# Kernel tuning notes

Hardware: AMD Instinct MI355X
Metric: run time of the kernel (lower is better)

Reference implementation:

```python
import jax, jax.numpy as jnp
import numpy as np

S, B, C = 7, 2, 20
LAMBDA_COORD, LAMBDA_NOOBJ = 5.0, 0.5
N_BATCH = 8192
OBJ_PROB = 0.05


def setup_inputs() -> dict:
    key = jax.random.key(0)
    k_pred, k_tgt, k_obj = jax.random.split(key, 3)
    pred = jax.random.normal(k_pred, (N_BATCH, S * S * (5 * B + C)), dtype=jnp.float32)
    # target cells: [conf, x, y, w, h, 20 class scores]; conf must be exactly 0/1
    tgt = jax.random.uniform(k_tgt, (N_BATCH * S * S, 5 + C), dtype=jnp.float32)
    obj = jax.random.bernoulli(k_obj, OBJ_PROB, (N_BATCH * S * S,)).astype(jnp.float32)
    tgt = tgt.at[:, 0].set(obj)
    target = tgt.reshape(N_BATCH, S * S * (5 + C))
    return {"pred": pred, "target": target}


def _to_xyxy(xywh, gy, gx):
    # xywh: [..., 4]; gy/gx broadcastable to leading dims
    cx = (gx + xywh[..., 0]) / S
    cy = (gy + xywh[..., 1]) / S
    w = xywh[..., 2]
    h = xywh[..., 3]
    return jnp.stack([cx - w / 2, cy - h / 2, cx + w / 2, cy + h / 2], axis=-1)


def _yolo_loss(pred, target):
    N = pred.shape[0]
    p = pred.reshape(-1, 5 * B + C)          # [M, 30], M = N*S*S
    t = target.reshape(-1, 5 + C)            # [M, 25]
    M = p.shape[0]
    objf = (t[:, 0] == 1.0).astype(p.dtype)
    noobjf = (t[:, 0] == 0.0).astype(p.dtype)

    boxes = p[:, : 5 * B].reshape(M, B, 5)   # [M, B, 5] (conf, x, y, w, h)
    tbox = t[:, :5]                           # [M, 5]

    grid = jnp.tile(jnp.arange(S * S), M // (S * S))
    gy = (grid // 7).astype(p.dtype)
    gx = (grid % 7).astype(p.dtype)

    # IoU matching (pred wh taken as abs, matching .square().sqrt())
    pb = jnp.abs(boxes[..., 1:5])                             # [M, B, 4]
    pxyxy = _to_xyxy(pb, gy[:, None], gx[:, None])            # [M, B, 4]
    txyxy = _to_xyxy(tbox[:, 1:5], gy, gx)                    # [M, 4]

    lt = jnp.maximum(pxyxy[..., :2], txyxy[:, None, :2])
    rb = jnp.minimum(pxyxy[..., 2:], txyxy[:, None, 2:])
    wh = jnp.clip(rb - lt, 0.0)
    inter = wh[..., 0] * wh[..., 1]                           # [M, B]
    area_p = (pxyxy[..., 2] - pxyxy[..., 0]) * (pxyxy[..., 3] - pxyxy[..., 1])
    area_t = (txyxy[..., 2] - txyxy[..., 0]) * (txyxy[..., 3] - txyxy[..., 1])
    iou = inter / (area_p + area_t[:, None] - inter)          # [M, B]

    best = jnp.argmax(iou, axis=1)                            # first max on ties, like torch
    max_iou = jnp.max(iou, axis=1)                            # [M]
    resp = jnp.take_along_axis(boxes, best[:, None, None], axis=1)[:, 0]  # [M, 5]

    # localization (raw pred xy; sqrt(abs(wh)))
    xy_loss = jnp.sum(objf[:, None] * (resp[:, 1:3] - tbox[:, 1:3]) ** 2)
    pw = jnp.sqrt(jnp.abs(resp[:, 3:5]))
    tw = jnp.sqrt(jnp.abs(tbox[:, 3:5]))
    wh_loss = jnp.sum(objf[:, None] * (pw - tw) ** 2)
    localization = LAMBDA_COORD * (xy_loss + wh_loss)

    # confidence: responsible box conf vs IoU (IoU NOT detached, as in source)
    obj_conf = jnp.sum(objf * (resp[:, 0] - max_iou) ** 2)
    noobj_conf = LAMBDA_NOOBJ * jnp.sum(noobjf[:, None] * boxes[:, :, 0] ** 2)

    cls_loss = jnp.sum(objf[:, None] * (p[:, -C:] - t[:, -C:]) ** 2)

    return (localization + obj_conf + noobj_conf + cls_loss) / N


def reference(pred, target):
    return _yolo_loss(pred, target)
```

## Files before the change

kernel.cpp:

```cpp
#include <hip/hip_runtime.h>


#define NBATCH  8192
#define PSTRIDE 30
#define TSTRIDE 25
#define TPB     256
#define NCHUNKS 1568

__global__ __launch_bounds__(TPB) void yolo_partial_kernel(
    const float* __restrict__ pred,
    const float* __restrict__ tgt,
    float* __restrict__ partials)
{
    __shared__ float sp[TPB * PSTRIDE];
    __shared__ float st[TPB * TSTRIDE];

    const int tid = threadIdx.x;
    const size_t c0 = (size_t)blockIdx.x * TPB;

    const float4* gp = (const float4*)(pred + c0 * PSTRIDE);
    float4* lp = (float4*)sp;
    #pragma unroll
    for (int k = 0; k < 7; ++k)
        lp[tid + k * TPB] = gp[tid + k * TPB];
    if (tid < 128)
        lp[tid + 7 * TPB] = gp[tid + 7 * TPB];

    const float4* gt = (const float4*)(tgt + c0 * TSTRIDE);
    float4* lt = (float4*)st;
    #pragma unroll
    for (int k = 0; k < 6; ++k)
        lt[tid + k * TPB] = gt[tid + k * TPB];
    if (tid < 64)
        lt[tid + 6 * TPB] = gt[tid + 6 * TPB];

    __syncthreads();

    const float* p = sp + tid * PSTRIDE;
    const float* t = st + tid * TSTRIDE;

    int cell = (int)((c0 + tid) % 49);
    float gy = (float)(cell / 7);
    float gx = (float)(cell % 7);
    const float invS = 1.0f / 7.0f;

    float t0 = t[0], tx = t[1], ty = t[2], tw = t[3], th = t[4];
    float objf   = (t0 == 1.0f) ? 1.0f : 0.0f;
    float noobjf = (t0 == 0.0f) ? 1.0f : 0.0f;

    float tcx = (gx + tx) * invS, tcy = (gy + ty) * invS;
    float tx1 = tcx - tw * 0.5f, ty1 = tcy - th * 0.5f;
    float tx2 = tcx + tw * 0.5f, ty2 = tcy + th * 0.5f;
    float area_t = (tx2 - tx1) * (ty2 - ty1);

    float conf[2], bx[2], by[2], bw[2], bh[2], iou[2];
    #pragma unroll
    for (int b = 0; b < 2; ++b) {
        conf[b] = p[b * 5 + 0];
        bx[b]   = p[b * 5 + 1];
        by[b]   = p[b * 5 + 2];
        bw[b]   = p[b * 5 + 3];
        bh[b]   = p[b * 5 + 4];
        float ax = fabsf(bx[b]), ay = fabsf(by[b]);
        float aw = fabsf(bw[b]), ah = fabsf(bh[b]);
        float cx = (gx + ax) * invS, cy = (gy + ay) * invS;
        float x1 = cx - aw * 0.5f, y1 = cy - ah * 0.5f;
        float x2 = cx + aw * 0.5f, y2 = cy + ah * 0.5f;
        float ltx = fmaxf(x1, tx1), lty = fmaxf(y1, ty1);
        float rbx = fminf(x2, tx2), rby = fminf(y2, ty2);
        float wx = fmaxf(rbx - ltx, 0.0f);
        float wy = fmaxf(rby - lty, 0.0f);
        float inter = wx * wy;
        float area_p = (x2 - x1) * (y2 - y1);
        iou[b] = inter / (area_p + area_t - inter);
    }

    int best = (iou[1] > iou[0]) ? 1 : 0;
    float miou = fmaxf(iou[0], iou[1]);

    float rc = conf[best];
    float rx = bx[best], ry = by[best], rw = bw[best], rh = bh[best];

    float dx = rx - tx, dy = ry - ty;
    float sw = sqrtf(fabsf(rw)) - sqrtf(fabsf(tw));
    float sh = sqrtf(fabsf(rh)) - sqrtf(fabsf(th));
    float loc = dx * dx + dy * dy + sw * sw + sh * sh;

    float oc = rc - miou;
    oc = oc * oc;

    float no = conf[0] * conf[0] + conf[1] * conf[1];

    float cls = 0.0f;
    #pragma unroll
    for (int k = 0; k < 20; ++k) {
        float d = p[10 + k] - t[5 + k];
        cls += d * d;
    }

    float part = objf * (5.0f * loc + oc + cls) + 0.5f * noobjf * no;

    #pragma unroll
    for (int off = 32; off > 0; off >>= 1)
        part += __shfl_down(part, off, 64);

    __shared__ float ws[4];
    int lane = tid & 63;
    int wid  = tid >> 6;
    if (lane == 0) ws[wid] = part;
    __syncthreads();
    if (tid == 0)
        partials[blockIdx.x] = ws[0] + ws[1] + ws[2] + ws[3];
}

__global__ __launch_bounds__(TPB) void yolo_final_kernel(
    const float* __restrict__ partials,
    float* __restrict__ out, float invN)
{
    const int tid = threadIdx.x;
    float s = 0.0f;
    for (int i = tid; i < NCHUNKS; i += TPB)
        s += partials[i];

    #pragma unroll
    for (int off = 32; off > 0; off >>= 1)
        s += __shfl_down(s, off, 64);

    __shared__ float ws[4];
    int lane = tid & 63;
    int wid  = tid >> 6;
    if (lane == 0) ws[wid] = s;
    __syncthreads();
    if (tid == 0)
        out[0] = (ws[0] + ws[1] + ws[2] + ws[3]) * invN;
}

extern "C" void kernel_launch(void* const* d_in, const int* in_sizes, int n_in,
                              void* d_out, int out_size, void* d_ws, size_t ws_size,
                              hipStream_t stream) {
    const float* pred = (const float*)d_in[0];
    const float* tgt  = (const float*)d_in[1];
    float* out = (float*)d_out;
    float* partials = (float*)d_ws;

    yolo_partial_kernel<<<NCHUNKS, TPB, 0, stream>>>(pred, tgt, partials);
    yolo_final_kernel<<<1, TPB, 0, stream>>>(partials, out, 1.0f / (float)NBATCH);
}
```

Baseline: 25.20 us.

## Fuse partial and final reduction into one cooperative kernel with grid sync

Replaces the two-kernel reduction with a single cooperatively launched, persistent grid-stride kernel. Each block accumulates over several chunks, writes a partial, then a grid-wide barrier lets block 0 do the final sum. This removes the second kernel launch and its launch gap. The costs are the cooperative launch, the grid barrier, an occupancy query on every call, and a grid capped by per-CU occupancy (with 55KB of shared memory only about two blocks fit per CU). The old two-kernel path stays as a fallback.

```diff
diff --git a/kernel.cpp b/kernel.cpp
--- a/kernel.cpp
+++ b/kernel.cpp
@@ -1,4 +1,7 @@
 #include <hip/hip_runtime.h>
+#include <hip/hip_cooperative_groups.h>
+
+namespace cg = cooperative_groups;
 
 
 #define NBATCH  8192
@@ -7,39 +10,10 @@
 #define TPB     256
 #define NCHUNKS 1568
 
-__global__ __launch_bounds__(TPB) void yolo_partial_kernel(
-    const float* __restrict__ pred,
-    const float* __restrict__ tgt,
-    float* __restrict__ partials)
-{
-    __shared__ float sp[TPB * PSTRIDE];
-    __shared__ float st[TPB * TSTRIDE];
-
-    const int tid = threadIdx.x;
-    const size_t c0 = (size_t)blockIdx.x * TPB;
-
-    const float4* gp = (const float4*)(pred + c0 * PSTRIDE);
-    float4* lp = (float4*)sp;
-    #pragma unroll
-    for (int k = 0; k < 7; ++k)
-        lp[tid + k * TPB] = gp[tid + k * TPB];
-    if (tid < 128)
-        lp[tid + 7 * TPB] = gp[tid + 7 * TPB];
-
-    const float4* gt = (const float4*)(tgt + c0 * TSTRIDE);
-    float4* lt = (float4*)st;
-    #pragma unroll
-    for (int k = 0; k < 6; ++k)
-        lt[tid + k * TPB] = gt[tid + k * TPB];
-    if (tid < 64)
-        lt[tid + 6 * TPB] = gt[tid + 6 * TPB];
-
-    __syncthreads();
-
-    const float* p = sp + tid * PSTRIDE;
-    const float* t = st + tid * TSTRIDE;
-
-    int cell = (int)((c0 + tid) % 49);
+__device__ __forceinline__ float cell_loss(const float* __restrict__ p,
+                                           const float* __restrict__ t,
+                                           int cell)
+{
     float gy = (float)(cell / 7);
     float gx = (float)(cell % 7);
     const float invS = 1.0f / 7.0f;
@@ -98,37 +72,130 @@
         cls += d * d;
     }
 
-    float part = objf * (5.0f * loc + oc + cls) + 0.5f * noobjf * no;
+    return objf * (5.0f * loc + oc + cls) + 0.5f * noobjf * no;
+}
+
+__global__ __launch_bounds__(TPB) void yolo_fused_kernel(
+    const float* __restrict__ pred,
+    const float* __restrict__ tgt,
+    float* __restrict__ out,
+    float* __restrict__ partials, float invN)
+{
+    __shared__ float sp[TPB * PSTRIDE];
+    __shared__ float st[TPB * TSTRIDE];
+    __shared__ float ws[4];
+
+    const int tid = threadIdx.x;
+    float part = 0.0f;
+
+    for (int c = blockIdx.x; c < NCHUNKS; c += gridDim.x) {
+        const size_t c0 = (size_t)c * TPB;
+
+        const float4* gp = (const float4*)(pred + c0 * PSTRIDE);
+        float4* lp = (float4*)sp;
+        #pragma unroll
+        for (int k = 0; k < 7; ++k)
+            lp[tid + k * TPB] = gp[tid + k * TPB];
+        if (tid < 128)
+            lp[tid + 7 * TPB] = gp[tid + 7 * TPB];
+
+        const float4* gt = (const float4*)(tgt + c0 * TSTRIDE);
+        float4* lt = (float4*)st;
+        #pragma unroll
+        for (int k = 0; k < 6; ++k)
+            lt[tid + k * TPB] = gt[tid + k * TPB];
+        if (tid < 64)
+            lt[tid + 6 * TPB] = gt[tid + 6 * TPB];
+
+        __syncthreads();
+
+        part += cell_loss(sp + tid * PSTRIDE, st + tid * TSTRIDE,
+                          (int)((c0 + tid) % 49));
+
+        __syncthreads();
+    }
 
     #pragma unroll
     for (int off = 32; off > 0; off >>= 1)
         part += __shfl_down(part, off, 64);
-
-    __shared__ float ws[4];
-    int lane = tid & 63;
-    int wid  = tid >> 6;
+    int lane = tid & 63, wid = tid >> 6;
     if (lane == 0) ws[wid] = part;
     __syncthreads();
     if (tid == 0)
         partials[blockIdx.x] = ws[0] + ws[1] + ws[2] + ws[3];
+
+    cg::this_grid().sync();
+
+    if (blockIdx.x == 0) {
+        float s = 0.0f;
+        for (int i = tid; i < (int)gridDim.x; i += TPB)
+            s += partials[i];
+        #pragma unroll
+        for (int off = 32; off > 0; off >>= 1)
+            s += __shfl_down(s, off, 64);
+        if (lane == 0) ws[wid] = s;
+        __syncthreads();
+        if (tid == 0)
+            out[0] = (ws[0] + ws[1] + ws[2] + ws[3]) * invN;
+    }
+}
+
+__global__ __launch_bounds__(TPB) void yolo_partial_kernel(
+    const float* __restrict__ pred,
+    const float* __restrict__ tgt,
+    float* __restrict__ partials)
+{
+    __shared__ float sp[TPB * PSTRIDE];
+    __shared__ float st[TPB * TSTRIDE];
+
+    const int tid = threadIdx.x;
+    const size_t c0 = (size_t)blockIdx.x * TPB;
+
+    const float4* gp = (const float4*)(pred + c0 * PSTRIDE);
+    float4* lp = (float4*)sp;
+    #pragma unroll
+    for (int k = 0; k < 7; ++k)
+        lp[tid + k * TPB] = gp[tid + k * TPB];
+    if (tid < 128)
+        lp[tid + 7 * TPB] = gp[tid + 7 * TPB];
+
+    const float4* gt = (const float4*)(tgt + c0 * TSTRIDE);
+    float4* lt = (float4*)st;
+    #pragma unroll
+    for (int k = 0; k < 6; ++k)
+        lt[tid + k * TPB] = gt[tid + k * TPB];
+    if (tid < 64)
+        lt[tid + 6 * TPB] = gt[tid + 6 * TPB];
+
+    __syncthreads();
+
+    float part = cell_loss(sp + tid * PSTRIDE, st + tid * TSTRIDE,
+                           (int)((c0 + tid) % 49));
+
+    #pragma unroll
+    for (int off = 32; off > 0; off >>= 1)
+        part += __shfl_down(part, off, 64);
+    __shared__ float ws[4];
+    int lane = tid & 63, wid = tid >> 6;
+    if (lane == 0) ws[wid] = part;
+    __syncthreads();
+    if (tid == 0)
+        partials[blockIdx.x] = ws[0] + ws[1] + ws[2] + ws[3];
 }
 
 __global__ __launch_bounds__(TPB) void yolo_final_kernel(
     const float* __restrict__ partials,
-    float* __restrict__ out, float invN)
+    float* __restrict__ out, float invN, int n)
 {
     const int tid = threadIdx.x;
     float s = 0.0f;
-    for (int i = tid; i < NCHUNKS; i += TPB)
+    for (int i = tid; i < n; i += TPB)
         s += partials[i];
-
     #pragma unroll
     for (int off = 32; off > 0; off >>= 1)
         s += __shfl_down(s, off, 64);
-
     __shared__ float ws[4];
-    int lane = tid & 63;
-    int wid  = tid >> 6;
+    int lane = tid & 63, wid = tid >> 6;
     if (lane == 0) ws[wid] = s;
     __syncthreads();
     if (tid == 0)
@@ -142,7 +209,23 @@
     const float* tgt  = (const float*)d_in[1];
     float* out = (float*)d_out;
     float* partials = (float*)d_ws;
+    float invN = 1.0f / (float)NBATCH;
+
+    int perCU = 0;
+    hipError_t e = hipOccupancyMaxActiveBlocksPerMultiprocessor(
+        &perCU, (const void*)yolo_fused_kernel, TPB, 0);
+
+    if (e == hipSuccess && perCU > 0) {
+        int grid = perCU * 256;
+        if (grid > NCHUNKS) grid = NCHUNKS;
+        void* args[] = {(void*)&pred, (void*)&tgt, (void*)&out,
+                        (void*)&partials, (void*)&invN};
+        hipError_t e2 = hipLaunchCooperativeKernel(
+            (const void*)yolo_fused_kernel, dim3(grid), dim3(TPB),
+            args, 0, stream);
+        if (e2 == hipSuccess) return;
+    }
 
     yolo_partial_kernel<<<NCHUNKS, TPB, 0, stream>>>(pred, tgt, partials);
-    yolo_final_kernel<<<1, TPB, 0, stream>>>(partials, out, 1.0f / (float)NBATCH);
-}
+    yolo_final_kernel<<<1, TPB, 0, stream>>>(partials, out, invN, NCHUNKS);
+}
```

Result: slower. 73.69 us (+192.5%).

## Fuse final reduction into partial kernel using per-block release/acquire flags

Applied to the files above, without the earlier changes.

Merges the two-kernel reduction into one launch. Each block writes its partial sum and then publishes a magic flag with release semantics. Block 0 spins on the flags with acquire loads and does the final sum, which removes the second kernel launch and its dependency gap. The flags are never reset between calls, so on a repeat call block 0 can read stale partials from the previous call. Block 0 also busy-waits for every other block, which relies on all blocks eventually being scheduled.

```diff
diff --git a/kernel.cpp b/kernel.cpp
--- a/kernel.cpp
+++ b/kernel.cpp
@@ -6,14 +6,19 @@
 #define TSTRIDE 25
 #define TPB     256
 #define NCHUNKS 1568
+#define MAGIC   0x3F8A2B1Cu
 
-__global__ __launch_bounds__(TPB) void yolo_partial_kernel(
+__global__ __launch_bounds__(TPB) void yolo_onepass_kernel(
     const float* __restrict__ pred,
     const float* __restrict__ tgt,
-    float* __restrict__ partials)
+    float* __restrict__ out,
+    float* __restrict__ partials,
+    unsigned int* __restrict__ flags,
+    float invN)
 {
     __shared__ float sp[TPB * PSTRIDE];
     __shared__ float st[TPB * TSTRIDE];
+    __shared__ float ws[4];
 
     const int tid = threadIdx.x;
     const size_t c0 = (size_t)blockIdx.x * TPB;
@@ -103,36 +108,33 @@
     #pragma unroll
     for (int off = 32; off > 0; off >>= 1)
         part += __shfl_down(part, off, 64);
-
-    __shared__ float ws[4];
-    int lane = tid & 63;
-    int wid  = tid >> 6;
+    int lane = tid & 63, wid = tid >> 6;
     if (lane == 0) ws[wid] = part;
     __syncthreads();
-    if (tid == 0)
+
+    if (tid == 0) {
         partials[blockIdx.x] = ws[0] + ws[1] + ws[2] + ws[3];
-}
+        __hip_atomic_store(&flags[blockIdx.x], MAGIC,
+                           __ATOMIC_RELEASE, __HIP_MEMORY_SCOPE_AGENT);
+    }
 
-__global__ __launch_bounds__(TPB) void yolo_final_kernel(
-    const float* __restrict__ partials,
-    float* __restrict__ out, float invN)
-{
-    const int tid = threadIdx.x;
-    float s = 0.0f;
-    for (int i = tid; i < NCHUNKS; i += TPB)
-        s += partials[i];
-
-    #pragma unroll
-    for (int off = 32; off > 0; off >>= 1)
-        s += __shfl_down(s, off, 64);
-
-    __shared__ float ws[4];
-    int lane = tid & 63;
-    int wid  = tid >> 6;
-    if (lane == 0) ws[wid] = s;
-    __syncthreads();
-    if (tid == 0)
-        out[0] = (ws[0] + ws[1] + ws[2] + ws[3]) * invN;
+    if (blockIdx.x == 0) {
+        float s = 0.0f;
+        for (int i = tid; i < NCHUNKS; i += TPB) {
+            while (__hip_atomic_load(&flags[i], __ATOMIC_ACQUIRE,
+                                     __HIP_MEMORY_SCOPE_AGENT) != MAGIC) {}
+            s += __hip_atomic_load(&partials[i], __ATOMIC_RELAXED,
+                                   __HIP_MEMORY_SCOPE_AGENT);
+        }
+        #pragma unroll
+        for (int off = 32; off > 0; off >>= 1)
+            s += __shfl_down(s, off, 64);
+        __syncthreads();
+        if (lane == 0) ws[wid] = s;
+        __syncthreads();
+        if (tid == 0)
+            out[0] = (ws[0] + ws[1] + ws[2] + ws[3]) * invN;
+    }
 }
 
 extern "C" void kernel_launch(void* const* d_in, const int* in_sizes, int n_in,
@@ -141,8 +143,10 @@
     const float* pred = (const float*)d_in[0];
     const float* tgt  = (const float*)d_in[1];
     float* out = (float*)d_out;
-    float* partials = (float*)d_ws;
 
-    yolo_partial_kernel<<<NCHUNKS, TPB, 0, stream>>>(pred, tgt, partials);
-    yolo_final_kernel<<<1, TPB, 0, stream>>>(partials, out, 1.0f / (float)NBATCH);
+    float* partials     = (float*)d_ws;
+    unsigned int* flags = (unsigned int*)((char*)d_ws + 8192);
+
+    yolo_onepass_kernel<<<NCHUNKS, TPB, 0, stream>>>(
+        pred, tgt, out, partials, flags, 1.0f / (float)NBATCH);
 }
```

Result: slower. 42.08 us (+67.0%).
